# Kernel optimization log

Hardware: AMD Instinct MI355X
Metric: run time of the kernel (lower is better)

## Reference

```python
import jax, jax.numpy as jnp
import numpy as np

N = 100000
E = 1600000
NEG_SLOPE = 0.2
EPS = 1e-16


def gat_conv(x, src, dst, W, att_src, att_dst, bias, num_nodes, concat):
    """PyG-style GATConv (eval mode, self-loops already appended by caller).
    x: [N, F_in]; W: [F_in, H*C]; att_src/att_dst: [H, C]; bias: [H*C] or [C].
    """
    H, C = att_src.shape
    h = (x @ W).reshape(num_nodes, H, C)              # [N, H, C]
    a_src = jnp.einsum('nhc,hc->nh', h, att_src)      # [N, H]
    a_dst = jnp.einsum('nhc,hc->nh', h, att_dst)      # [N, H]
    alpha = jax.nn.leaky_relu(a_src[src] + a_dst[dst], NEG_SLOPE)  # [E, H]
    # segment softmax over incoming edges of each destination node
    amax = jax.ops.segment_max(alpha, dst, num_segments=num_nodes)  # [N, H]
    alpha = jnp.exp(alpha - amax[dst])
    asum = jax.ops.segment_sum(alpha, dst, num_segments=num_nodes)  # [N, H]
    alpha = alpha / (asum[dst] + EPS)
    # weighted aggregation: scatter-add messages to destination nodes
    out = jax.ops.segment_sum(h[src] * alpha[:, :, None], dst, num_segments=num_nodes)  # [N, H, C]
    if concat:
        out = out.reshape(num_nodes, H * C)
    else:
        out = out.mean(axis=1)
    return out + bias


def setup_inputs() -> dict:
    key = jax.random.key(0)
    ks = jax.random.split(key, 12)
    in_ch, hid, out_ch, nhead = 1024, 8, 19, 16
    x = jax.random.normal(ks[0], (N, in_ch), dtype=jnp.float32)
    edge_index = jax.random.randint(ks[1], (2, E), 0, N, dtype=jnp.int32)
    g = 0.1
    return {
        'x': x,
        'edge_index': edge_index,
        'W1': jax.random.normal(ks[2], (in_ch, nhead * hid), dtype=jnp.float32) * g,
        'att_src1': jax.random.normal(ks[3], (nhead, hid), dtype=jnp.float32) * g,
        'att_dst1': jax.random.normal(ks[4], (nhead, hid), dtype=jnp.float32) * g,
        'b1': jnp.zeros((nhead * hid,), dtype=jnp.float32),
        'W2': jax.random.normal(ks[5], (nhead * hid, 1 * out_ch), dtype=jnp.float32) * g,
        'att_src2': jax.random.normal(ks[6], (1, out_ch), dtype=jnp.float32) * g,
        'att_dst2': jax.random.normal(ks[7], (1, out_ch), dtype=jnp.float32) * g,
        'b2': jnp.zeros((out_ch,), dtype=jnp.float32),
    }


def reference(x, edge_index, W1, att_src1, att_dst1, b1, W2, att_src2, att_dst2, b2):
    # eval mode: all dropout layers are identity
    # PyG GATConv adds self-loops by default
    loop = jnp.arange(N, dtype=edge_index.dtype)
    src = jnp.concatenate([edge_index[0], loop])
    dst = jnp.concatenate([edge_index[1], loop])
    h = jax.nn.elu(gat_conv(x, src, dst, W1, att_src1, att_dst1, b1, N, concat=True))
    h = gat_conv(h, src, dst, W2, att_src2, att_dst2, b2, N, concat=False)
    return jax.nn.log_softmax(h, axis=1)
```

## Files before the change

### kernel.cpp

```cpp
#include <hip/hip_runtime.h>
#include <math.h>

#define NN 100000
#define EE 1600000
#define ET (EE + NN)
#define F1 128
#define NH 16
#define F2 19

typedef __bf16 bf16x8 __attribute__((ext_vector_type(8)));
typedef float f32x4 __attribute__((ext_vector_type(4)));

#define LDST 40

__global__ __launch_bounds__(256) void deg_kernel(const int* __restrict__ dst, int* __restrict__ deg) {
  int e = blockIdx.x * 256 + threadIdx.x;
  if (e >= ET) return;
  int d = (e < EE) ? dst[e] : (e - EE);
  atomicAdd(&deg[d], 1);
}

#define SCB 391
__global__ __launch_bounds__(256) void scan_block(const int* __restrict__ deg, int* __restrict__ offs,
                                                  int* __restrict__ bsum) {
  __shared__ int wsum[4];
  int b = blockIdx.x, tid = threadIdx.x;
  int i = b * 256 + tid;
  int lane = tid & 63, wid = tid >> 6;
  int v = (i < NN) ? deg[i] : 0;
  int x = v;
  #pragma unroll
  for (int off = 1; off < 64; off <<= 1) {
    int t = __shfl_up(x, off, 64);
    if (lane >= off) x += t;
  }
  if (lane == 63) wsum[wid] = x;
  __syncthreads();
  int add = 0;
  #pragma unroll
  for (int w = 0; w < 4; ++w) if (w < wid) add += wsum[w];
  if (i < NN) offs[i] = x + add - v;
  if (tid == 255) bsum[b] = x + add;
}

__global__ __launch_bounds__(512) void scan_tops(int* __restrict__ bsum, int* __restrict__ tops,
                                                 int* __restrict__ offs) {
  __shared__ int wsum[8];
  int tid = threadIdx.x;
  int lane = tid & 63, wid = tid >> 6;
  int v = (tid < SCB) ? bsum[tid] : 0;
  int x = v;
  #pragma unroll
  for (int off = 1; off < 64; off <<= 1) {
    int t = __shfl_up(x, off, 64);
    if (lane >= off) x += t;
  }
  if (lane == 63) wsum[wid] = x;
  __syncthreads();
  int add = 0;
  #pragma unroll
  for (int w = 0; w < 8; ++w) if (w < wid) add += wsum[w];
  if (tid < SCB) tops[tid] = x + add - v;
  if (tid == SCB - 1) offs[NN] = x + add;
}

__global__ __launch_bounds__(256) void scan_add(int* __restrict__ offs, const int* __restrict__ tops) {
  int i = blockIdx.x * 256 + threadIdx.x;
  if (i < NN) offs[i] += tops[blockIdx.x];
}

__global__ __launch_bounds__(256) void fill_kernel(const int* __restrict__ src, const int* __restrict__ dst,
                                                   const int* __restrict__ offs, int* __restrict__ cnt,
                                                   int* __restrict__ csr) {
  int e = blockIdx.x * 256 + threadIdx.x;
  if (e >= ET) return;
  int d, s;
  if (e < EE) { d = dst[e]; s = src[e]; } else { d = e - EE; s = e - EE; }
  int pos = offs[d] + atomicAdd(&cnt[d], 1);
  csr[pos] = s;
}

__global__ __launch_bounds__(256) void wsplit_kernel(const float* __restrict__ W, __bf16* __restrict__ Wth,
                                                     __bf16* __restrict__ Wtl) {
  int idx = blockIdx.x * 256 + threadIdx.x;
  if (idx >= 1024 * 128) return;
  int k = idx >> 7, n = idx & 127;
  float v = W[idx];
  __bf16 h = (__bf16)v;
  __bf16 l = (__bf16)(v - (float)h);
  Wth[(size_t)n * 1024 + k] = h;
  Wtl[(size_t)n * 1024 + k] = l;
}

__global__ __launch_bounds__(256) void gemm1_mfma(const float* __restrict__ X, const __bf16* __restrict__ Wth,
                                                  const __bf16* __restrict__ Wtl, float* __restrict__ H1, int M) {
  __shared__ __bf16 Ah[128 * LDST];
  __shared__ __bf16 Al[128 * LDST];
  __shared__ __bf16 Bh[128 * LDST];
  __shared__ __bf16 Bl[128 * LDST];
  const int tid = threadIdx.x;
  const int m0 = blockIdx.x * 128;
  const int wv = tid >> 6, lane = tid & 63;
  const int lrow = lane & 15, quad = lane >> 4;
  const int sr = tid >> 1;
  const int sk = (tid & 1) * 16;
  int grow = m0 + sr; if (grow > M - 1) grow = M - 1;
  const float* xrow = &X[(size_t)grow * 1024];
  const __bf16* wthr = &Wth[(size_t)sr * 1024];
  const __bf16* wtlr = &Wtl[(size_t)sr * 1024];

  f32x4 acc[2][8];
  #pragma unroll
  for (int i = 0; i < 2; ++i)
    #pragma unroll
    for (int j = 0; j < 8; ++j) acc[i][j] = (f32x4){0.f, 0.f, 0.f, 0.f};

  for (int k0 = 0; k0 < 1024; k0 += 32) {
    float tmp[16];
    {
      const float4 v0 = *reinterpret_cast<const float4*>(&xrow[k0 + sk + 0]);
      const float4 v1 = *reinterpret_cast<const float4*>(&xrow[k0 + sk + 4]);
      const float4 v2 = *reinterpret_cast<const float4*>(&xrow[k0 + sk + 8]);
      const float4 v3 = *reinterpret_cast<const float4*>(&xrow[k0 + sk + 12]);
      tmp[0] = v0.x; tmp[1] = v0.y; tmp[2] = v0.z; tmp[3] = v0.w;
      tmp[4] = v1.x; tmp[5] = v1.y; tmp[6] = v1.z; tmp[7] = v1.w;
      tmp[8] = v2.x; tmp[9] = v2.y; tmp[10] = v2.z; tmp[11] = v2.w;
      tmp[12] = v3.x; tmp[13] = v3.y; tmp[14] = v3.z; tmp[15] = v3.w;
    }
    bf16x8 hv0, hv1, lv0, lv1;
    #pragma unroll
    for (int j = 0; j < 8; ++j) {
      __bf16 h = (__bf16)tmp[j];
      hv0[j] = h; lv0[j] = (__bf16)(tmp[j] - (float)h);
    }
    #pragma unroll
    for (int j = 0; j < 8; ++j) {
      __bf16 h = (__bf16)tmp[8 + j];
      hv1[j] = h; lv1[j] = (__bf16)(tmp[8 + j] - (float)h);
    }
    *reinterpret_cast<bf16x8*>(&Ah[sr * LDST + sk]) = hv0;
    *reinterpret_cast<bf16x8*>(&Ah[sr * LDST + sk + 8]) = hv1;
    *reinterpret_cast<bf16x8*>(&Al[sr * LDST + sk]) = lv0;
    *reinterpret_cast<bf16x8*>(&Al[sr * LDST + sk + 8]) = lv1;
    {
      bf16x8 b0 = *reinterpret_cast<const bf16x8*>(&wthr[k0 + sk]);
      bf16x8 b1 = *reinterpret_cast<const bf16x8*>(&wthr[k0 + sk + 8]);
      bf16x8 c0 = *reinterpret_cast<const bf16x8*>(&wtlr[k0 + sk]);
      bf16x8 c1 = *reinterpret_cast<const bf16x8*>(&wtlr[k0 + sk + 8]);
      *reinterpret_cast<bf16x8*>(&Bh[sr * LDST + sk]) = b0;
      *reinterpret_cast<bf16x8*>(&Bh[sr * LDST + sk + 8]) = b1;
      *reinterpret_cast<bf16x8*>(&Bl[sr * LDST + sk]) = c0;
      *reinterpret_cast<bf16x8*>(&Bl[sr * LDST + sk + 8]) = c1;
    }
    __syncthreads();
    bf16x8 afh[2], afl[2];
    #pragma unroll
    for (int mt = 0; mt < 2; ++mt) {
      int r = wv * 32 + mt * 16 + lrow;
      afh[mt] = *reinterpret_cast<const bf16x8*>(&Ah[r * LDST + quad * 8]);
      afl[mt] = *reinterpret_cast<const bf16x8*>(&Al[r * LDST + quad * 8]);
    }
    #pragma unroll
    for (int nt = 0; nt < 8; ++nt) {
      int r = nt * 16 + lrow;
      bf16x8 bfh = *reinterpret_cast<const bf16x8*>(&Bh[r * LDST + quad * 8]);
      bf16x8 bfl = *reinterpret_cast<const bf16x8*>(&Bl[r * LDST + quad * 8]);
      #pragma unroll
      for (int mt = 0; mt < 2; ++mt) {
        acc[mt][nt] = __builtin_amdgcn_mfma_f32_16x16x32_bf16(afh[mt], bfh, acc[mt][nt], 0, 0, 0);
        acc[mt][nt] = __builtin_amdgcn_mfma_f32_16x16x32_bf16(afl[mt], bfh, acc[mt][nt], 0, 0, 0);
        acc[mt][nt] = __builtin_amdgcn_mfma_f32_16x16x32_bf16(afh[mt], bfl, acc[mt][nt], 0, 0, 0);
      }
    }
    __syncthreads();
  }
  #pragma unroll
  for (int mt = 0; mt < 2; ++mt) {
    #pragma unroll
    for (int r = 0; r < 4; ++r) {
      int row = m0 + wv * 32 + mt * 16 + quad * 4 + r;
      if (row < M) {
        #pragma unroll
        for (int nt = 0; nt < 8; ++nt) {
          H1[(size_t)row * 128 + nt * 16 + lrow] = acc[mt][nt][r];
        }
      }
    }
  }
}

__global__ __launch_bounds__(256) void a1_kernel(const float* __restrict__ h1, const float* __restrict__ att_s,
                                                 const float* __restrict__ att_d, float* __restrict__ a_src,
                                                 float* __restrict__ a_dst) {
  int idx = blockIdx.x * 256 + threadIdx.x;
  if (idx >= NN * NH) return;
  int h = idx & 15;
  const float4 v0 = *reinterpret_cast<const float4*>(&h1[(size_t)idx * 8]);
  const float4 v1 = *reinterpret_cast<const float4*>(&h1[(size_t)idx * 8 + 4]);
  const float4 s0 = *reinterpret_cast<const float4*>(&att_s[h * 8]);
  const float4 s1 = *reinterpret_cast<const float4*>(&att_s[h * 8 + 4]);
  const float4 d0 = *reinterpret_cast<const float4*>(&att_d[h * 8]);
  const float4 d1 = *reinterpret_cast<const float4*>(&att_d[h * 8 + 4]);
  float s = v0.x * s0.x + v0.y * s0.y + v0.z * s0.z + v0.w * s0.w
          + v1.x * s1.x + v1.y * s1.y + v1.z * s1.z + v1.w * s1.w;
  float d = v0.x * d0.x + v0.y * d0.y + v0.z * d0.z + v0.w * d0.w
          + v1.x * d1.x + v1.y * d1.y + v1.z * d1.z + v1.w * d1.w;
  a_src[idx] = s; a_dst[idx] = d;
}

__global__ __launch_bounds__(256) void agg1_kernel(const float* __restrict__ h1, const float* __restrict__ a_src,
                                                   const float* __restrict__ a_dst, const int* __restrict__ offs,
                                                   const int* __restrict__ csr, const float* __restrict__ b1,
                                                   float* __restrict__ act1) {
  const int wid = threadIdx.x >> 6, lane = threadIdx.x & 63;
  const int n = blockIdx.x * 4 + wid;
  if (n >= NN) return;
  const int beg = offs[n], end = offs[n + 1];
  const int h = lane >> 2;
  const int c2 = lane * 2;
  const float adst = a_dst[n * NH + h];
  float2 acc0 = {0.f, 0.f}, acc1 = {0.f, 0.f}, acc2 = {0.f, 0.f}, acc3 = {0.f, 0.f};
  float ls0 = 0.f, ls1 = 0.f, ls2 = 0.f, ls3 = 0.f;
  int e = beg;
  for (; e + 3 < end; e += 4) {
    int s0 = csr[e], s1 = csr[e + 1], s2 = csr[e + 2], s3 = csr[e + 3];
    float a0 = a_src[s0 * NH + h] + adst;
    float a1 = a_src[s1 * NH + h] + adst;
    float a2 = a_src[s2 * NH + h] + adst;
    float a3 = a_src[s3 * NH + h] + adst;
    a0 = a0 > 0.f ? a0 : 0.2f * a0;
    a1 = a1 > 0.f ? a1 : 0.2f * a1;
    a2 = a2 > 0.f ? a2 : 0.2f * a2;
    a3 = a3 > 0.f ? a3 : 0.2f * a3;
    float w0 = __expf(a0), w1 = __expf(a1), w2 = __expf(a2), w3 = __expf(a3);
    float2 hv0 = *reinterpret_cast<const float2*>(&h1[(size_t)s0 * 128 + c2]);
    float2 hv1 = *reinterpret_cast<const float2*>(&h1[(size_t)s1 * 128 + c2]);
    float2 hv2 = *reinterpret_cast<const float2*>(&h1[(size_t)s2 * 128 + c2]);
    float2 hv3 = *reinterpret_cast<const float2*>(&h1[(size_t)s3 * 128 + c2]);
    ls0 += w0; ls1 += w1; ls2 += w2; ls3 += w3;
    acc0.x += w0 * hv0.x; acc0.y += w0 * hv0.y;
    acc1.x += w1 * hv1.x; acc1.y += w1 * hv1.y;
    acc2.x += w2 * hv2.x; acc2.y += w2 * hv2.y;
    acc3.x += w3 * hv3.x; acc3.y += w3 * hv3.y;
  }
  for (; e < end; ++e) {
    int s0 = csr[e];
    float a0 = a_src[s0 * NH + h] + adst;
    a0 = a0 > 0.f ? a0 : 0.2f * a0;
    float w0 = __expf(a0);
    float2 hv0 = *reinterpret_cast<const float2*>(&h1[(size_t)s0 * 128 + c2]);
    ls0 += w0;
    acc0.x += w0 * hv0.x; acc0.y += w0 * hv0.y;
  }
  float lsum = (ls0 + ls1) + (ls2 + ls3);
  float inv = 1.f / (lsum + 1e-16f);
  float ox = ((acc0.x + acc1.x) + (acc2.x + acc3.x)) * inv + b1[c2];
  float oy = ((acc0.y + acc1.y) + (acc2.y + acc3.y)) * inv + b1[c2 + 1];
  float2 o;
  o.x = ox > 0.f ? ox : expm1f(ox);
  o.y = oy > 0.f ? oy : expm1f(oy);
  *reinterpret_cast<float2*>(&act1[(size_t)n * 128 + c2]) = o;
}

__global__ __launch_bounds__(256) void gemm2_kernel(const float* __restrict__ A, const float* __restrict__ W2,
                                                    float* __restrict__ H2) {
  __shared__ float Ws[128 * 19];
  for (int i = threadIdx.x; i < 128 * 19; i += 256) Ws[i] = W2[i];
  __syncthreads();
  int idx = blockIdx.x * 256 + threadIdx.x;
  if (idx >= NN * F2) return;
  int row = idx / F2, col = idx % F2;
  const float* a = &A[(size_t)row * 128];
  float s = 0.f;
  #pragma unroll 8
  for (int k = 0; k < 128; ++k) s += a[k] * Ws[k * F2 + col];
  H2[idx] = s;
}

__global__ __launch_bounds__(256) void a2_kernel(const float* __restrict__ h2, const float* __restrict__ att_s,
                                                 const float* __restrict__ att_d, float* __restrict__ a_src,
                                                 float* __restrict__ a_dst) {
  int n = blockIdx.x * 256 + threadIdx.x;
  if (n >= NN) return;
  const float* hp = &h2[(size_t)n * F2];
  float s = 0.f, d = 0.f;
  #pragma unroll
  for (int c = 0; c < F2; ++c) {
    float v = hp[c];
    s += v * att_s[c];
    d += v * att_d[c];
  }
  a_src[n] = s; a_dst[n] = d;
}

__global__ __launch_bounds__(256) void agg2_kernel(const float* __restrict__ h2, const float* __restrict__ a_src,
                                                   const float* __restrict__ a_dst, const int* __restrict__ offs,
                                                   const int* __restrict__ csr, const float* __restrict__ b2,
                                                   float* __restrict__ out) {
  const int wid = threadIdx.x >> 6, lane = threadIdx.x & 63;
  const int n = blockIdx.x * 4 + wid;
  if (n >= NN) return;
  const int beg = offs[n], end = offs[n + 1];
  const float adst = a_dst[n];
  const int g = lane / 19;
  const int c = lane - g * 19;
  float acc = 0.f, ls = 0.f;
  if (g < 3) {
    int e = beg + g;
    for (; e + 3 < end; e += 6) {
      int s0 = csr[e], s1 = csr[e + 3];
      float a0 = a_src[s0] + adst;
      float a1 = a_src[s1] + adst;
      a0 = a0 > 0.f ? a0 : 0.2f * a0;
      a1 = a1 > 0.f ? a1 : 0.2f * a1;
      float w0 = __expf(a0), w1 = __expf(a1);
      float v0 = h2[(size_t)s0 * F2 + c];
      float v1 = h2[(size_t)s1 * F2 + c];
      ls += w0 + w1;
      acc += w0 * v0 + w1 * v1;
    }
    if (e < end) {
      int s0 = csr[e];
      float a0 = a_src[s0] + adst;
      a0 = a0 > 0.f ? a0 : 0.2f * a0;
      float w0 = __expf(a0);
      ls += w0;
      acc += w0 * h2[(size_t)s0 * F2 + c];
    }
  }
  float acc_t = __shfl(acc, c, 64) + __shfl(acc, c + 19, 64) + __shfl(acc, c + 38, 64);
  float ls_t  = __shfl(ls, c, 64) + __shfl(ls, c + 19, 64) + __shfl(ls, c + 38, 64);
  const bool act = lane < F2;
  float o = acc_t / (ls_t + 1e-16f) + (act ? b2[lane] : 0.f);
  float v = act ? o : -INFINITY;
  float mx = v;
  #pragma unroll
  for (int off = 16; off >= 1; off >>= 1) mx = fmaxf(mx, __shfl_xor(mx, off, 32));
  float se = act ? __expf(v - mx) : 0.f;
  float sum = se;
  #pragma unroll
  for (int off = 16; off >= 1; off >>= 1) sum += __shfl_xor(sum, off, 32);
  if (act) out[(size_t)n * F2 + lane] = (o - mx) - logf(sum);
}

extern "C" void kernel_launch(void* const* d_in, const int* in_sizes, int n_in,
                              void* d_out, int out_size, void* d_ws, size_t ws_size,
                              hipStream_t stream) {
  const float* x   = (const float*)d_in[0];
  const int* ei    = (const int*)d_in[1];
  const float* W1  = (const float*)d_in[2];
  const float* as1 = (const float*)d_in[3];
  const float* ad1 = (const float*)d_in[4];
  const float* b1  = (const float*)d_in[5];
  const float* W2  = (const float*)d_in[6];
  const float* as2 = (const float*)d_in[7];
  const float* ad2 = (const float*)d_in[8];
  const float* b2  = (const float*)d_in[9];
  float* out = (float*)d_out;

  const int* srcp = ei;
  const int* dstp = ei + EE;

  char* p = (char*)d_ws;
  auto alloc = [&](size_t bytes) { char* r = p; p += (bytes + 255) & ~(size_t)255; return r; };
  float* h1    = (float*)alloc((size_t)NN * F1 * 4);
  float* act1  = (float*)alloc((size_t)NN * F1 * 4);
  float* a_s1  = (float*)alloc((size_t)NN * NH * 4);
  float* a_d1  = (float*)alloc((size_t)NN * NH * 4);
  float* h2    = (float*)alloc((size_t)NN * F2 * 4);
  float* a_s2  = (float*)alloc((size_t)NN * 4);
  float* a_d2  = (float*)alloc((size_t)NN * 4);
  int*   deg   = (int*)alloc((size_t)NN * 4);
  int*   offs  = (int*)alloc((size_t)(NN + 1) * 4);
  int*   cnt   = (int*)alloc((size_t)NN * 4);
  int*   csr   = (int*)alloc((size_t)ET * 4);
  int*   bsum  = (int*)alloc((size_t)SCB * 4);
  int*   tops  = (int*)alloc((size_t)SCB * 4);
  __bf16* Wth  = (__bf16*)alloc((size_t)128 * 1024 * 2);
  __bf16* Wtl  = (__bf16*)alloc((size_t)128 * 1024 * 2);

  hipMemsetAsync(deg, 0, (size_t)NN * 4, stream);
  hipMemsetAsync(cnt, 0, (size_t)NN * 4, stream);

  int eb = (ET + 255) / 256;
  deg_kernel<<<eb, 256, 0, stream>>>(dstp, deg);
  scan_block<<<SCB, 256, 0, stream>>>(deg, offs, bsum);
  scan_tops<<<1, 512, 0, stream>>>(bsum, tops, offs);
  scan_add<<<SCB, 256, 0, stream>>>(offs, tops);
  fill_kernel<<<eb, 256, 0, stream>>>(srcp, dstp, offs, cnt, csr);

  wsplit_kernel<<<(1024 * 128 + 255) / 256, 256, 0, stream>>>(W1, Wth, Wtl);
  gemm1_mfma<<<(NN + 127) / 128, 256, 0, stream>>>(x, Wth, Wtl, h1, NN);
  a1_kernel<<<(NN * NH + 255) / 256, 256, 0, stream>>>(h1, as1, ad1, a_s1, a_d1);
  agg1_kernel<<<(NN + 3) / 4, 256, 0, stream>>>(h1, a_s1, a_d1, offs, csr, b1, act1);

  gemm2_kernel<<<(NN * F2 + 255) / 256, 256, 0, stream>>>(act1, W2, h2);
  a2_kernel<<<(NN + 255) / 256, 256, 0, stream>>>(h2, as2, ad2, a_s2, a_d2);
  agg2_kernel<<<(NN + 3) / 4, 256, 0, stream>>>(h2, a_s2, a_d2, offs, csr, b2, out);
}
```

Baseline: 1.049 ms.

## Load GEMM A fragments directly to registers and store intermediates in fp16

The first GEMM now loads X rows straight into registers in MFMA fragment layout, prefetching the next k-slice, and splits them into bf16 hi/lo there. This drops the A-side shared-memory staging and its split pass. Separately, the gathered features h1, the layer-1 activations and h2 are stored in fp16, roughly halving the bytes moved in the gather-heavy aggregation kernels and the second GEMM. The cost is reduced precision in the intermediates. The GEMM's global reads of X are also less coalesced, since each lane now reads 32-byte pieces from many rows.

```diff
diff --git a/kernel.cpp b/kernel.cpp
--- a/kernel.cpp
+++ b/kernel.cpp
@@ -10,6 +10,8 @@
 
 typedef __bf16 bf16x8 __attribute__((ext_vector_type(8)));
 typedef float f32x4 __attribute__((ext_vector_type(4)));
+typedef _Float16 f16x2 __attribute__((ext_vector_type(2)));
+typedef _Float16 f16x8 __attribute__((ext_vector_type(8)));
 
 #define LDST 40
 
@@ -94,8 +96,6 @@
 
 __global__ __launch_bounds__(256) void gemm1_mfma(const float* __restrict__ X, const __bf16* __restrict__ Wth,
                                                   const __bf16* __restrict__ Wtl, float* __restrict__ H1, int M) {
-  __shared__ __bf16 Ah[128 * LDST];
-  __shared__ __bf16 Al[128 * LDST];
   __shared__ __bf16 Bh[128 * LDST];
   __shared__ __bf16 Bl[128 * LDST];
   const int tid = threadIdx.x;
@@ -104,10 +104,16 @@
   const int lrow = lane & 15, quad = lane >> 4;
   const int sr = tid >> 1;
   const int sk = (tid & 1) * 16;
-  int grow = m0 + sr; if (grow > M - 1) grow = M - 1;
-  const float* xrow = &X[(size_t)grow * 1024];
   const __bf16* wthr = &Wth[(size_t)sr * 1024];
   const __bf16* wtlr = &Wtl[(size_t)sr * 1024];
+
+  const float* arow[2];
+  #pragma unroll
+  for (int mt = 0; mt < 2; ++mt) {
+    int r = m0 + wv * 32 + mt * 16 + lrow;
+    if (r > M - 1) r = M - 1;
+    arow[mt] = &X[(size_t)r * 1024 + quad * 8];
+  }
 
   f32x4 acc[2][8];
   #pragma unroll
@@ -115,33 +121,14 @@
     #pragma unroll
     for (int j = 0; j < 8; ++j) acc[i][j] = (f32x4){0.f, 0.f, 0.f, 0.f};
 
+  float4 av0[2], av1[2];
+  #pragma unroll
+  for (int mt = 0; mt < 2; ++mt) {
+    av0[mt] = *reinterpret_cast<const float4*>(&arow[mt][0]);
+    av1[mt] = *reinterpret_cast<const float4*>(&arow[mt][4]);
+  }
+
   for (int k0 = 0; k0 < 1024; k0 += 32) {
-    float tmp[16];
-    {
-      const float4 v0 = *reinterpret_cast<const float4*>(&xrow[k0 + sk + 0]);
-      const float4 v1 = *reinterpret_cast<const float4*>(&xrow[k0 + sk + 4]);
-      const float4 v2 = *reinterpret_cast<const float4*>(&xrow[k0 + sk + 8]);
-      const float4 v3 = *reinterpret_cast<const float4*>(&xrow[k0 + sk + 12]);
-      tmp[0] = v0.x; tmp[1] = v0.y; tmp[2] = v0.z; tmp[3] = v0.w;
-      tmp[4] = v1.x; tmp[5] = v1.y; tmp[6] = v1.z; tmp[7] = v1.w;
-      tmp[8] = v2.x; tmp[9] = v2.y; tmp[10] = v2.z; tmp[11] = v2.w;
-      tmp[12] = v3.x; tmp[13] = v3.y; tmp[14] = v3.z; tmp[15] = v3.w;
-    }
-    bf16x8 hv0, hv1, lv0, lv1;
-    #pragma unroll
-    for (int j = 0; j < 8; ++j) {
-      __bf16 h = (__bf16)tmp[j];
-      hv0[j] = h; lv0[j] = (__bf16)(tmp[j] - (float)h);
-    }
-    #pragma unroll
-    for (int j = 0; j < 8; ++j) {
-      __bf16 h = (__bf16)tmp[8 + j];
-      hv1[j] = h; lv1[j] = (__bf16)(tmp[8 + j] - (float)h);
-    }
-    *reinterpret_cast<bf16x8*>(&Ah[sr * LDST + sk]) = hv0;
-    *reinterpret_cast<bf16x8*>(&Ah[sr * LDST + sk + 8]) = hv1;
-    *reinterpret_cast<bf16x8*>(&Al[sr * LDST + sk]) = lv0;
-    *reinterpret_cast<bf16x8*>(&Al[sr * LDST + sk + 8]) = lv1;
     {
       bf16x8 b0 = *reinterpret_cast<const bf16x8*>(&wthr[k0 + sk]);
       bf16x8 b1 = *reinterpret_cast<const bf16x8*>(&wthr[k0 + sk + 8]);
@@ -152,14 +139,26 @@
       *reinterpret_cast<bf16x8*>(&Bl[sr * LDST + sk]) = c0;
       *reinterpret_cast<bf16x8*>(&Bl[sr * LDST + sk + 8]) = c1;
     }
-    __syncthreads();
     bf16x8 afh[2], afl[2];
     #pragma unroll
     for (int mt = 0; mt < 2; ++mt) {
-      int r = wv * 32 + mt * 16 + lrow;
-      afh[mt] = *reinterpret_cast<const bf16x8*>(&Ah[r * LDST + quad * 8]);
-      afl[mt] = *reinterpret_cast<const bf16x8*>(&Al[r * LDST + quad * 8]);
-    }
+      float t[8] = {av0[mt].x, av0[mt].y, av0[mt].z, av0[mt].w,
+                    av1[mt].x, av1[mt].y, av1[mt].z, av1[mt].w};
+      #pragma unroll
+      for (int j = 0; j < 8; ++j) {
+        __bf16 h = (__bf16)t[j];
+        afh[mt][j] = h;
+        afl[mt][j] = (__bf16)(t[j] - (float)h);
+      }
+    }
+    if (k0 + 32 < 1024) {
+      #pragma unroll
+      for (int mt = 0; mt < 2; ++mt) {
+        av0[mt] = *reinterpret_cast<const float4*>(&arow[mt][k0 + 32]);
+        av1[mt] = *reinterpret_cast<const float4*>(&arow[mt][k0 + 36]);
+      }
+    }
+    __syncthreads();
     #pragma unroll
     for (int nt = 0; nt < 8; ++nt) {
       int r = nt * 16 + lrow;
@@ -191,7 +190,7 @@
 
 __global__ __launch_bounds__(256) void a1_kernel(const float* __restrict__ h1, const float* __restrict__ att_s,
                                                  const float* __restrict__ att_d, float* __restrict__ a_src,
-                                                 float* __restrict__ a_dst) {
+                                                 float* __restrict__ a_dst, _Float16* __restrict__ h1h) {
   int idx = blockIdx.x * 256 + threadIdx.x;
   if (idx >= NN * NH) return;
   int h = idx & 15;
@@ -206,12 +205,16 @@
   float d = v0.x * d0.x + v0.y * d0.y + v0.z * d0.z + v0.w * d0.w
           + v1.x * d1.x + v1.y * d1.y + v1.z * d1.z + v1.w * d1.w;
   a_src[idx] = s; a_dst[idx] = d;
-}
-
-__global__ __launch_bounds__(256) void agg1_kernel(const float* __restrict__ h1, const float* __restrict__ a_src,
+  f16x8 hv;
+  hv[0] = (_Float16)v0.x; hv[1] = (_Float16)v0.y; hv[2] = (_Float16)v0.z; hv[3] = (_Float16)v0.w;
+  hv[4] = (_Float16)v1.x; hv[5] = (_Float16)v1.y; hv[6] = (_Float16)v1.z; hv[7] = (_Float16)v1.w;
+  *reinterpret_cast<f16x8*>(&h1h[(size_t)idx * 8]) = hv;
+}
+
+__global__ __launch_bounds__(256) void agg1_kernel(const _Float16* __restrict__ h1h, const float* __restrict__ a_src,
                                                    const float* __restrict__ a_dst, const int* __restrict__ offs,
                                                    const int* __restrict__ csr, const float* __restrict__ b1,
-                                                   float* __restrict__ act1) {
+                                                   _Float16* __restrict__ act1) {
   const int wid = threadIdx.x >> 6, lane = threadIdx.x & 63;
   const int n = blockIdx.x * 4 + wid;
   if (n >= NN) return;
@@ -233,67 +236,71 @@
     a2 = a2 > 0.f ? a2 : 0.2f * a2;
     a3 = a3 > 0.f ? a3 : 0.2f * a3;
     float w0 = __expf(a0), w1 = __expf(a1), w2 = __expf(a2), w3 = __expf(a3);
-    float2 hv0 = *reinterpret_cast<const float2*>(&h1[(size_t)s0 * 128 + c2]);
-    float2 hv1 = *reinterpret_cast<const float2*>(&h1[(size_t)s1 * 128 + c2]);
-    float2 hv2 = *reinterpret_cast<const float2*>(&h1[(size_t)s2 * 128 + c2]);
-    float2 hv3 = *reinterpret_cast<const float2*>(&h1[(size_t)s3 * 128 + c2]);
+    f16x2 hv0 = *reinterpret_cast<const f16x2*>(&h1h[(size_t)s0 * 128 + c2]);
+    f16x2 hv1 = *reinterpret_cast<const f16x2*>(&h1h[(size_t)s1 * 128 + c2]);
+    f16x2 hv2 = *reinterpret_cast<const f16x2*>(&h1h[(size_t)s2 * 128 + c2]);
+    f16x2 hv3 = *reinterpret_cast<const f16x2*>(&h1h[(size_t)s3 * 128 + c2]);
     ls0 += w0; ls1 += w1; ls2 += w2; ls3 += w3;
-    acc0.x += w0 * hv0.x; acc0.y += w0 * hv0.y;
-    acc1.x += w1 * hv1.x; acc1.y += w1 * hv1.y;
-    acc2.x += w2 * hv2.x; acc2.y += w2 * hv2.y;
-    acc3.x += w3 * hv3.x; acc3.y += w3 * hv3.y;
+    acc0.x += w0 * (float)hv0[0]; acc0.y += w0 * (float)hv0[1];
+    acc1.x += w1 * (float)hv1[0]; acc1.y += w1 * (float)hv1[1];
+    acc2.x += w2 * (float)hv2[0]; acc2.y += w2 * (float)hv2[1];
+    acc3.x += w3 * (float)hv3[0]; acc3.y += w3 * (float)hv3[1];
   }
   for (; e < end; ++e) {
     int s0 = csr[e];
     float a0 = a_src[s0 * NH + h] + adst;
     a0 = a0 > 0.f ? a0 : 0.2f * a0;
     float w0 = __expf(a0);
-    float2 hv0 = *reinterpret_cast<const float2*>(&h1[(size_t)s0 * 128 + c2]);
+    f16x2 hv0 = *reinterpret_cast<const f16x2*>(&h1h[(size_t)s0 * 128 + c2]);
     ls0 += w0;
-    acc0.x += w0 * hv0.x; acc0.y += w0 * hv0.y;
+    acc0.x += w0 * (float)hv0[0]; acc0.y += w0 * (float)hv0[1];
   }
   float lsum = (ls0 + ls1) + (ls2 + ls3);
   float inv = 1.f / (lsum + 1e-16f);
   float ox = ((acc0.x + acc1.x) + (acc2.x + acc3.x)) * inv + b1[c2];
   float oy = ((acc0.y + acc1.y) + (acc2.y + acc3.y)) * inv + b1[c2 + 1];
-  float2 o;
-  o.x = ox > 0.f ? ox : expm1f(ox);
-  o.y = oy > 0.f ? oy : expm1f(oy);
-  *reinterpret_cast<float2*>(&act1[(size_t)n * 128 + c2]) = o;
-}
-
-__global__ __launch_bounds__(256) void gemm2_kernel(const float* __restrict__ A, const float* __restrict__ W2,
-                                                    float* __restrict__ H2) {
+  ox = ox > 0.f ? ox : expm1f(ox);
+  oy = oy > 0.f ? oy : expm1f(oy);
+  f16x2 o;
+  o[0] = (_Float16)ox; o[1] = (_Float16)oy;
+  *reinterpret_cast<f16x2*>(&act1[(size_t)n * 128 + c2]) = o;
+}
+
+__global__ __launch_bounds__(256) void gemm2_kernel(const _Float16* __restrict__ A, const float* __restrict__ W2,
+                                                    _Float16* __restrict__ H2) {
   __shared__ float Ws[128 * 19];
   for (int i = threadIdx.x; i < 128 * 19; i += 256) Ws[i] = W2[i];
   __syncthreads();
   int idx = blockIdx.x * 256 + threadIdx.x;
   if (idx >= NN * F2) return;
   int row = idx / F2, col = idx % F2;
-  const float* a = &A[(size_t)row * 128];
+  const f16x2* a = reinterpret_cast<const f16x2*>(&A[(size_t)row * 128]);
   float s = 0.f;
   #pragma unroll 8
-  for (int k = 0; k < 128; ++k) s += a[k] * Ws[k * F2 + col];
-  H2[idx] = s;
-}
-
-__global__ __launch_bounds__(256) void a2_kernel(const float* __restrict__ h2, const float* __restrict__ att_s,
+  for (int k = 0; k < 64; ++k) {
+    f16x2 v = a[k];
+    s += (float)v[0] * Ws[(2 * k) * F2 + col] + (float)v[1] * Ws[(2 * k + 1) * F2 + col];
+  }
+  H2[idx] = (_Float16)s;
+}
+
+__global__ __launch_bounds__(256) void a2_kernel(const _Float16* __restrict__ h2, const float* __restrict__ att_s,
                                                  const float* __restrict__ att_d, float* __restrict__ a_src,
                                                  float* __restrict__ a_dst) {
   int n = blockIdx.x * 256 + threadIdx.x;
   if (n >= NN) return;
-  const float* hp = &h2[(size_t)n * F2];
+  const _Float16* hp = &h2[(size_t)n * F2];
   float s = 0.f, d = 0.f;
   #pragma unroll
   for (int c = 0; c < F2; ++c) {
-    float v = hp[c];
+    float v = (float)hp[c];
     s += v * att_s[c];
     d += v * att_d[c];
   }
   a_src[n] = s; a_dst[n] = d;
 }
 
-__global__ __launch_bounds__(256) void agg2_kernel(const float* __restrict__ h2, const float* __restrict__ a_src,
+__global__ __launch_bounds__(256) void agg2_kernel(const _Float16* __restrict__ h2, const float* __restrict__ a_src,
                                                    const float* __restrict__ a_dst, const int* __restrict__ offs,
                                                    const int* __restrict__ csr, const float* __restrict__ b2,
                                                    float* __restrict__ out) {
@@ -314,8 +321,8 @@
       a0 = a0 > 0.f ? a0 : 0.2f * a0;
       a1 = a1 > 0.f ? a1 : 0.2f * a1;
       float w0 = __expf(a0), w1 = __expf(a1);
-      float v0 = h2[(size_t)s0 * F2 + c];
-      float v1 = h2[(size_t)s1 * F2 + c];
+      float v0 = (float)h2[(size_t)s0 * F2 + c];
+      float v1 = (float)h2[(size_t)s1 * F2 + c];
       ls += w0 + w1;
       acc += w0 * v0 + w1 * v1;
     }
@@ -325,7 +332,7 @@
       a0 = a0 > 0.f ? a0 : 0.2f * a0;
       float w0 = __expf(a0);
       ls += w0;
-      acc += w0 * h2[(size_t)s0 * F2 + c];
+      acc += w0 * (float)h2[(size_t)s0 * F2 + c];
     }
   }
   float acc_t = __shfl(acc, c, 64) + __shfl(acc, c + 19, 64) + __shfl(acc, c + 38, 64);
@@ -363,21 +370,22 @@
 
   char* p = (char*)d_ws;
   auto alloc = [&](size_t bytes) { char* r = p; p += (bytes + 255) & ~(size_t)255; return r; };
-  float* h1    = (float*)alloc((size_t)NN * F1 * 4);
-  float* act1  = (float*)alloc((size_t)NN * F1 * 4);
-  float* a_s1  = (float*)alloc((size_t)NN * NH * 4);
-  float* a_d1  = (float*)alloc((size_t)NN * NH * 4);
-  float* h2    = (float*)alloc((size_t)NN * F2 * 4);
-  float* a_s2  = (float*)alloc((size_t)NN * 4);
-  float* a_d2  = (float*)alloc((size_t)NN * 4);
-  int*   deg   = (int*)alloc((size_t)NN * 4);
-  int*   offs  = (int*)alloc((size_t)(NN + 1) * 4);
-  int*   cnt   = (int*)alloc((size_t)NN * 4);
-  int*   csr   = (int*)alloc((size_t)ET * 4);
-  int*   bsum  = (int*)alloc((size_t)SCB * 4);
-  int*   tops  = (int*)alloc((size_t)SCB * 4);
-  __bf16* Wth  = (__bf16*)alloc((size_t)128 * 1024 * 2);
-  __bf16* Wtl  = (__bf16*)alloc((size_t)128 * 1024 * 2);
+  float*    h1    = (float*)alloc((size_t)NN * F1 * 4);
+  _Float16* h1h   = (_Float16*)alloc((size_t)NN * F1 * 2);
+  _Float16* act1h = (_Float16*)alloc((size_t)NN * F1 * 2);
+  float*    a_s1  = (float*)alloc((size_t)NN * NH * 4);
+  float*    a_d1  = (float*)alloc((size_t)NN * NH * 4);
+  _Float16* h2h   = (_Float16*)alloc((size_t)NN * F2 * 2);
+  float*    a_s2  = (float*)alloc((size_t)NN * 4);
+  float*    a_d2  = (float*)alloc((size_t)NN * 4);
+  int*      deg   = (int*)alloc((size_t)NN * 4);
+  int*      offs  = (int*)alloc((size_t)(NN + 1) * 4);
+  int*      cnt   = (int*)alloc((size_t)NN * 4);
+  int*      csr   = (int*)alloc((size_t)ET * 4);
+  int*      bsum  = (int*)alloc((size_t)SCB * 4);
+  int*      tops  = (int*)alloc((size_t)SCB * 4);
+  __bf16*   Wth   = (__bf16*)alloc((size_t)128 * 1024 * 2);
+  __bf16*   Wtl   = (__bf16*)alloc((size_t)128 * 1024 * 2);
 
   hipMemsetAsync(deg, 0, (size_t)NN * 4, stream);
   hipMemsetAsync(cnt, 0, (size_t)NN * 4, stream);
@@ -391,10 +399,10 @@
 
   wsplit_kernel<<<(1024 * 128 + 255) / 256, 256, 0, stream>>>(W1, Wth, Wtl);
   gemm1_mfma<<<(NN + 127) / 128, 256, 0, stream>>>(x, Wth, Wtl, h1, NN);
-  a1_kernel<<<(NN * NH + 255) / 256, 256, 0, stream>>>(h1, as1, ad1, a_s1, a_d1);
-  agg1_kernel<<<(NN + 3) / 4, 256, 0, stream>>>(h1, a_s1, a_d1, offs, csr, b1, act1);
-
-  gemm2_kernel<<<(NN * F2 + 255) / 256, 256, 0, stream>>>(act1, W2, h2);
-  a2_kernel<<<(NN + 255) / 256, 256, 0, stream>>>(h2, as2, ad2, a_s2, a_d2);
-  agg2_kernel<<<(NN + 3) / 4, 256, 0, stream>>>(h2, a_s2, a_d2, offs, csr, b2, out);
-}
+  a1_kernel<<<(NN * NH + 255) / 256, 256, 0, stream>>>(h1, as1, ad1, a_s1, a_d1, h1h);
+  agg1_kernel<<<(NN + 3) / 4, 256, 0, stream>>>(h1h, a_s1, a_d1, offs, csr, b1, act1h);
+
+  gemm2_kernel<<<(NN * F2 + 255) / 256, 256, 0, stream>>>(act1h, W2, h2h);
+  a2_kernel<<<(NN + 255) / 256, 256, 0, stream>>>(h2h, as2, ad2, a_s2, a_d2);
+  agg2_kernel<<<(NN + 3) / 4, 256, 0, stream>>>(h2h, a_s2, a_d2, offs, csr, b2, out);
+}
```

New measurement: 966.0 us. 7.9% less time.
